# Kernel tuning notes

Measured on AMD Instinct MI355X. Metric: run time of the kernel, lower is better.

Reference implementation:

```python
import jax, jax.numpy as jnp
import numpy as np

B, S, D, H = 2, 2048, 1024, 16
DH = D // H
LEVELS, FACTOR = 3, 2


def setup_inputs() -> dict:
    key = jax.random.key(0)
    ks = jax.random.split(key, 12)
    s = 1.0 / np.sqrt(D)
    n = lambda k, shape, sc: (jax.random.normal(k, shape, jnp.float32) * sc)
    return {
        "query": n(ks[0], (B, S, D), 1.0),
        "key": n(ks[1], (B, S, D), 1.0),
        "value": n(ks[2], (B, S, D), 1.0),
        "Wq": n(ks[3], (D, D), s), "bq": jnp.zeros((D,), jnp.float32),
        "Wk": n(ks[4], (D, D), s), "bk": jnp.zeros((D,), jnp.float32),
        "Wv": n(ks[5], (D, D), s), "bv": jnp.zeros((D,), jnp.float32),
        "Wo": n(ks[6], (D, D), s), "bo": jnp.zeros((D,), jnp.float32),
        "w_levels": jnp.ones((LEVELS,), jnp.float32),
    }


def _downsample(m):
    # mean-pool pairs along sequence: [B, S, D] -> [B, S//FACTOR, D]
    b, s, d = m.shape
    sn = s // FACTOR
    return m[:, : sn * FACTOR, :].reshape(b, sn, FACTOR, d).mean(axis=2)


def _mha(q, k, v, Wq, bq, Wk, bk, Wv, bv, Wo, bo):
    b, sq, d = q.shape
    sk = k.shape[1]
    qh = (q @ Wq + bq).reshape(b, sq, H, DH)
    kh = (k @ Wk + bk).reshape(b, sk, H, DH)
    vh = (v @ Wv + bv).reshape(b, sk, H, DH)
    scores = jnp.einsum("bqhd,bkhd->bhqk", qh, kh) / np.sqrt(DH)
    attn = jax.nn.softmax(scores, axis=-1)
    out = jnp.einsum("bhqk,bkhd->bqhd", attn, vh).reshape(b, sq, d)
    return out @ Wo + bo


def reference(query, key, value, Wq, bq, Wk, bk, Wv, bv, Wo, bo, w_levels):
    keys, vals = [key], [value]
    k_, v_ = key, value
    for _ in range(LEVELS - 1):
        k_ = _downsample(k_)
        v_ = _downsample(v_)
        keys.append(k_)
        vals.append(v_)
    acc = None
    for lvl in range(LEVELS):
        o = _mha(query, keys[lvl], vals[lvl], Wq, bq, Wk, bk, Wv, bv, Wo, bo)
        o = o * w_levels[lvl]
        acc = o if acc is None else acc + o
    return acc / w_levels.sum()
```

## Files before the change

### kernel.cpp

```cpp
#include <hip/hip_runtime.h>


#define B_  2
#define S_  2048
#define D_  1024
#define H_  16
#define DH_ 64
#define THR2 10.0f

typedef short s8v __attribute__((ext_vector_type(8)));
typedef float f4v __attribute__((ext_vector_type(4)));
typedef float f16v __attribute__((ext_vector_type(16)));
typedef unsigned int u32x2 __attribute__((ext_vector_type(2)));
typedef unsigned int u32x4 __attribute__((ext_vector_type(4)));

__device__ __forceinline__ unsigned cvtpk(float lo, float hi){
    unsigned r;
    asm volatile("v_cvt_pk_bf16_f32 %0, %1, %2" : "=v"(r) : "v"(lo), "v"(hi));
    return r;
}
__device__ __forceinline__ unsigned short f2bf1(float v){
    unsigned r;
    asm volatile("v_cvt_pk_bf16_f32 %0, %1, %2" : "=v"(r) : "v"(v), "v"(v));
    return (unsigned short)r;
}
__device__ __forceinline__ float bf2f(unsigned short h){
    union { unsigned u; float f; } v; v.u = ((unsigned)h) << 16;
    return v.f;
}
__device__ __forceinline__ float exp2_(float x){
    float r; asm("v_exp_f32 %0, %1" : "=v"(r) : "v"(x)); return r;
}
__device__ __forceinline__ float max3_(float a, float b, float c){
    float r; asm("v_max3_f32 %0, %1, %2, %3" : "=v"(r) : "v"(a), "v"(b), "v"(c));
    return r;
}
__device__ __forceinline__ void pswap(unsigned &dst, unsigned &src){
    asm volatile("v_permlane32_swap_b32 %0, %1" : "+v"(dst), "+v"(src));
}
__device__ __forceinline__ unsigned addpk3(unsigned x, unsigned y, unsigned z){
    union { unsigned u; float f; } xl, yl, zl, xh, yh, zh;
    xl.u = x << 16;          yl.u = y << 16;          zl.u = z << 16;
    xh.u = x & 0xFFFF0000u;  yh.u = y & 0xFFFF0000u;  zh.u = z & 0xFFFF0000u;
    return cvtpk(xl.f + yl.f + zl.f, xh.f + yh.f + zh.f);
}
__device__ __forceinline__ int swz(int row, int kb){
    return row*128 + (((kb) ^ (row & 7) ^ ((row >> 3) & 7)) << 4);
}
__device__ __forceinline__ void gld16(const void* g, void* l){
    __builtin_amdgcn_global_load_lds(
        (const __attribute__((address_space(1))) unsigned int*)g,
        (__attribute__((address_space(3))) unsigned int*)l, 16, 0, 0);
}

__global__ __launch_bounds__(256) void wtrans(
    const float* __restrict__ W0, const float* __restrict__ W1,
    const float* __restrict__ W2, const float* __restrict__ W3,
    unsigned short* __restrict__ T0, unsigned short* __restrict__ T1,
    unsigned short* __restrict__ T2, unsigned short* __restrict__ T3)
{
    __shared__ float tl[32][33];
    const float* W = blockIdx.z==0?W0: blockIdx.z==1?W1: blockIdx.z==2?W2:W3;
    unsigned short* T = blockIdx.z==0?T0: blockIdx.z==1?T1: blockIdx.z==2?T2:T3;
    const int t = threadIdx.x;
    const int bk = blockIdx.x*32, bn = blockIdx.y*32;
    {
        int row = t>>3, c4 = (t&7)*4;
        float4 v = *(const float4*)&W[(size_t)(bk+row)*D_ + bn + c4];
        tl[row][c4+0]=v.x; tl[row][c4+1]=v.y; tl[row][c4+2]=v.z; tl[row][c4+3]=v.w;
    }
    __syncthreads();
    {
        int n = t>>3, k4 = (t&7)*4;
        unsigned a = cvtpk(tl[k4+0][n], tl[k4+1][n]);
        unsigned b = cvtpk(tl[k4+2][n], tl[k4+3][n]);
        u32x2 pk = {a, b};
        *(u32x2*)&T[(size_t)(bn+n)*D_ + bk + k4] = pk;
    }
}

__global__ __launch_bounds__(256) void gemm_qkv3(
    const float* __restrict__ Aq, const float* __restrict__ Ak, const float* __restrict__ Avv,
    const unsigned short* __restrict__ Wq_, const unsigned short* __restrict__ Wk_,
    const unsigned short* __restrict__ Wv_,
    const float* __restrict__ bq_, const float* __restrict__ bk_, const float* __restrict__ bv_,
    unsigned short* __restrict__ Oq, unsigned short* __restrict__ Ok,
    unsigned short* __restrict__ Ov,
    unsigned short* __restrict__ K1, unsigned short* __restrict__ K2,
    float scale_q)
{
    const int z = blockIdx.z;
    const float* Af = z==0?Aq : z==1?Ak : Avv;
    const unsigned short* Btw = z==0?Wq_ : z==1?Wk_ : Wv_;
    const float* bias = z==0?bq_ : z==1?bk_ : bv_;
    unsigned short* C = z==0?Oq : z==1?Ok : Ov;
    const float scale = z==0? scale_q : 1.0f;

    const int N_ = D_, K_ = D_;
    __shared__ __align__(16) char lds[65536];
    const int t = threadIdx.x;
    const int l = t & 63, wvi = t>>6, g = l>>4, x = l&15;
    const int wr = wvi>>1, wc = wvi&1;
    const int br = blockIdx.x*128, bc = blockIdx.y*128;

    int rw[4], bl[4];
    #pragma unroll
    for (int p=0;p<4;++p){ int u = t + 256*p; rw[p] = u>>3; bl[p] = u&7; }

    f4v acc[4][4];
    #pragma unroll
    for (int i=0;i<4;++i)
        #pragma unroll
        for (int j=0;j<4;++j) acc[i][j] = (f4v){0.f,0.f,0.f,0.f};

    float4 alo[4], ahi[4]; s8v brg[4];
    #pragma unroll
    for (int p=0;p<4;++p){
        const float* ap = Af + (size_t)(br+rw[p])*K_ + bl[p]*8;
        alo[p] = *(const float4*)ap; ahi[p] = *(const float4*)(ap+4);
        brg[p] = *(const s8v*)(Btw + (size_t)(bc+rw[p])*K_ + bl[p]*8);
    }

    int cur = 0;
    for (int kt=0; kt<K_; kt+=64){
        char* AsB = lds + cur*32768;
        char* BsB = AsB + 16384;
        #pragma unroll
        for (int p=0;p<4;++p){
            uint4 pk;
            pk.x = cvtpk(alo[p].x, alo[p].y); pk.y = cvtpk(alo[p].z, alo[p].w);
            pk.z = cvtpk(ahi[p].x, ahi[p].y); pk.w = cvtpk(ahi[p].z, ahi[p].w);
            *(uint4*)(AsB + swz(rw[p], bl[p])) = pk;
            *(s8v*)(BsB + swz(rw[p], bl[p])) = brg[p];
        }
        if (kt + 64 < K_){
            #pragma unroll
            for (int p=0;p<4;++p){
                const float* ap = Af + (size_t)(br+rw[p])*K_ + (kt+64) + bl[p]*8;
                alo[p] = *(const float4*)ap; ahi[p] = *(const float4*)(ap+4);
                brg[p] = *(const s8v*)(Btw + (size_t)(bc+rw[p])*K_ + (kt+64) + bl[p]*8);
            }
        }
        __syncthreads();
        #pragma unroll
        for (int c=0;c<2;++c){
            s8v af[4], bf[4];
            #pragma unroll
            for (int fm=0; fm<4; ++fm)
                af[fm] = *(const s8v*)(AsB + swz(wr*64+fm*16+x, c*4+g));
            #pragma unroll
            for (int fn=0; fn<4; ++fn)
                bf[fn] = *(const s8v*)(BsB + swz(wc*64+fn*16+x, c*4+g));
            __builtin_amdgcn_s_setprio(1);
            #pragma unroll
            for (int fm=0; fm<4; ++fm)
                #pragma unroll
                for (int fn=0; fn<4; ++fn)
                    acc[fm][fn] = __builtin_amdgcn_mfma_f32_16x16x32_bf16(
                        af[fm], bf[fn], acc[fm][fn], 0,0,0);
            __builtin_amdgcn_s_setprio(0);
        }
        cur ^= 1;
    }

    #pragma unroll
    for (int fn=0; fn<4; ++fn){
        int col = bc + wc*64 + fn*16 + x;
        float bv = bias[col];
        #pragma unroll
        for (int fm=0; fm<4; ++fm){
            int row0 = br + wr*64 + fm*16 + g*4;
            float v0 = acc[fm][fn][0] + bv;
            float v1 = acc[fm][fn][1] + bv;
            float v2 = acc[fm][fn][2] + bv;
            float v3 = acc[fm][fn][3] + bv;
            int bI = row0>>11, sI = row0 & (S_-1);
            int hI = col>>6,  dhI = col & (DH_-1);
            size_t bh = (size_t)(bI*H_ + hI);
            if (z != 2){
                unsigned short* p0 = C + (bh*S_ + sI)*DH_ + dhI;
                p0[0]      = f2bf1(v0*scale);
                p0[DH_]    = f2bf1(v1*scale);
                p0[2*DH_]  = f2bf1(v2*scale);
                p0[3*DH_]  = f2bf1(v3*scale);
                if (z == 1){
                    unsigned short* p1 = K1 + (bh*(S_/2) + (sI>>1))*DH_ + dhI;
                    p1[0]   = f2bf1((v0+v1)*0.5f);
                    p1[DH_] = f2bf1((v2+v3)*0.5f);
                    K2[(bh*(S_/4) + (sI>>2))*DH_ + dhI] = f2bf1((v0+v1+v2+v3)*0.25f);
                }
            } else {
                u32x2 pk;
                pk.x = cvtpk(v0, v1);
                pk.y = cvtpk(v2, v3);
                *(u32x2*)&C[(bh*DH_+dhI)*S_ + sI] = pk;
            }
        }
    }
}

__global__ __launch_bounds__(256) void pool_v(
    const unsigned short* __restrict__ V0, unsigned short* __restrict__ V1,
    unsigned short* __restrict__ V2)
{
    int idx = blockIdx.x * 256 + threadIdx.x;
    int row = idx >> 8;
    int c8  = idx & 255;
    union { u32x4 u; unsigned short hh[8]; } a;
    a.u = *(const u32x4*)&V0[((size_t)row << 11) + c8*8];
    float m01 = 0.5f*(bf2f(a.hh[0])+bf2f(a.hh[1]));
    float m23 = 0.5f*(bf2f(a.hh[2])+bf2f(a.hh[3]));
    float m45 = 0.5f*(bf2f(a.hh[4])+bf2f(a.hh[5]));
    float m67 = 0.5f*(bf2f(a.hh[6])+bf2f(a.hh[7]));
    u32x2 p1; p1.x = cvtpk(m01, m23); p1.y = cvtpk(m45, m67);
    *(u32x2*)&V1[((size_t)row << 10) + c8*4] = p1;
    *(unsigned*)&V2[((size_t)row << 9) + c8*2] =
        cvtpk(0.5f*(m01+m23), 0.5f*(m45+m67));
}

__global__ __launch_bounds__(256) void gemm_sum(
    const unsigned short* __restrict__ A0, const unsigned short* __restrict__ A1,
    const unsigned short* __restrict__ A2, const unsigned short* __restrict__ Btw,
    const float* __restrict__ bias, float* __restrict__ C)
{
    const int N_ = D_, K_ = D_;
    __shared__ __align__(16) char lds[49152];
    const int t = threadIdx.x;
    const int l = t & 63, wvi = t>>6, g = l>>4, x = l&15;
    const int wr = wvi>>1, wc = wvi&1;
    const int br = blockIdx.x*128, bc = blockIdx.y*64;

    int rw[4], bl[4];
    #pragma unroll
    for (int p=0;p<4;++p){ int u = t + 256*p; rw[p] = u>>3; bl[p] = u&7; }
    int bw[2], bb[2];
    #pragma unroll
    for (int p=0;p<2;++p){ int u = t + 256*p; bw[p] = u>>3; bb[p] = u&7; }

    f4v acc[4][2];
    #pragma unroll
    for (int i=0;i<4;++i){ acc[i][0] = (f4v){0,0,0,0}; acc[i][1] = (f4v){0,0,0,0}; }

    u32x4 a0r[4], a1r[4], a2r[4]; s8v brg[2];
    #pragma unroll
    for (int p=0;p<4;++p){
        size_t off = (size_t)(br+rw[p])*K_ + bl[p]*8;
        a0r[p] = *(const u32x4*)(A0 + off);
        a1r[p] = *(const u32x4*)(A1 + off);
        a2r[p] = *(const u32x4*)(A2 + off);
    }
    #pragma unroll
    for (int p=0;p<2;++p)
        brg[p] = *(const s8v*)(Btw + (size_t)(bc+bw[p])*K_ + bb[p]*8);

    int cur = 0;
    for (int kt=0; kt<K_; kt+=64){
        char* AsB = lds + cur*24576;
        char* BsB = AsB + 16384;
        #pragma unroll
        for (int p=0;p<4;++p){
            uint4 pk;
            pk.x = addpk3(a0r[p].x, a1r[p].x, a2r[p].x);
            pk.y = addpk3(a0r[p].y, a1r[p].y, a2r[p].y);
            pk.z = addpk3(a0r[p].z, a1r[p].z, a2r[p].z);
            pk.w = addpk3(a0r[p].w, a1r[p].w, a2r[p].w);
            *(uint4*)(AsB + swz(rw[p], bl[p])) = pk;
        }
        #pragma unroll
        for (int p=0;p<2;++p)
            *(s8v*)(BsB + swz(bw[p], bb[p])) = brg[p];
        if (kt + 64 < K_){
            #pragma unroll
            for (int p=0;p<4;++p){
                size_t off = (size_t)(br+rw[p])*K_ + (kt+64) + bl[p]*8;
                a0r[p] = *(const u32x4*)(A0 + off);
                a1r[p] = *(const u32x4*)(A1 + off);
                a2r[p] = *(const u32x4*)(A2 + off);
            }
            #pragma unroll
            for (int p=0;p<2;++p)
                brg[p] = *(const s8v*)(Btw + (size_t)(bc+bw[p])*K_ + (kt+64) + bb[p]*8);
        }
        __syncthreads();
        #pragma unroll
        for (int c=0;c<2;++c){
            s8v af[4], bf[2];
            #pragma unroll
            for (int fm=0; fm<4; ++fm)
                af[fm] = *(const s8v*)(AsB + swz(wr*64+fm*16+x, c*4+g));
            #pragma unroll
            for (int fn=0; fn<2; ++fn)
                bf[fn] = *(const s8v*)(BsB + swz(wc*32+fn*16+x, c*4+g));
            __builtin_amdgcn_s_setprio(1);
            #pragma unroll
            for (int fm=0; fm<4; ++fm)
                #pragma unroll
                for (int fn=0; fn<2; ++fn)
                    acc[fm][fn] = __builtin_amdgcn_mfma_f32_16x16x32_bf16(
                        af[fm], bf[fn], acc[fm][fn], 0,0,0);
            __builtin_amdgcn_s_setprio(0);
        }
        cur ^= 1;
    }

    #pragma unroll
    for (int fn=0; fn<2; ++fn){
        int col = bc + wc*32 + fn*16 + x;
        float bv = bias[col];
        #pragma unroll
        for (int fm=0; fm<4; ++fm){
            int row0 = br + wr*64 + fm*16 + g*4;
            #pragma unroll
            for (int r=0;r<4;++r)
                C[(size_t)(row0+r)*N_ + col] = acc[fm][fn][r] + bv;
        }
    }
}

__global__ __launch_bounds__(256, 4) void attn_mfma11(
    const unsigned short* __restrict__ qh,
    const unsigned short* __restrict__ kh0, const unsigned short* __restrict__ kh1,
    const unsigned short* __restrict__ kh2,
    const unsigned short* __restrict__ vt0, const unsigned short* __restrict__ vt1,
    const unsigned short* __restrict__ vt2,
    const float* __restrict__ wlv,
    unsigned short* __restrict__ acc0, unsigned short* __restrict__ acc1,
    unsigned short* __restrict__ acc2)
{
    __shared__ __align__(16) char ldsA[32768];
    const int t = threadIdx.x, l = t&63, wv = t>>6, q = l&31, hi = l>>5;
    const int bh_ = blockIdx.x;
    const int h = bh_ & (H_-1), b = bh_ >> 4;
    const int qt = blockIdx.y;
    const int lvl = blockIdx.z;
    const int nt = 32 >> lvl;
    const unsigned short* kp  = lvl==0 ? kh0 : (lvl==1 ? kh1 : kh2);
    const unsigned short* vpt = lvl==0 ? vt0 : (lvl==1 ? vt1 : vt2);
    unsigned short* accOut    = lvl==0 ? acc0 : (lvl==1 ? acc1 : acc2);

    const float w0 = wlv[0], w1 = wlv[1], w2 = wlv[2];
    const float wl = wlv[lvl] / (w0 + w1 + w2);

    const unsigned short* qp =
        qh + (((size_t)(b*H_+h))*S_ + (size_t)qt*128 + wv*32 + q)*DH_ + hi*8;
    s8v qf0 = *(const s8v*)(qp);
    s8v qf1 = *(const s8v*)(qp + 16);
    s8v qf2 = *(const s8v*)(qp + 32);
    s8v qf3 = *(const s8v*)(qp + 48);

    const int Sl = nt*64;
    const char* gK = (const char*)(kp + (size_t)(b*H_+h)*Sl*DH_);
    const char* gV = (const char*)(vpt + (size_t)(b*H_+h)*DH_*Sl);

    const int lr = l>>3, lc = l&7;
    const int kb0 = lc ^ lr ^ wv;
    const int kb1 = lc ^ lr ^ (wv+4);
    const int kOffG0 = (((wv*8+lr)*DH_)    + kb0*8)*2;
    const int kOffG1 = (((32+wv*8+lr)*DH_) + kb1*8)*2;
    const int vOffG0 = ((wv*8+lr)*Sl    + kb0*8)*2;
    const int vOffG1 = ((32+wv*8+lr)*Sl + kb1*8)*2;
    const int ldsOff0 = wv*1024, ldsOff1 = 4096 + wv*1024;

    float m_i = -1e30f, l_i = 0.f;
    f16v o0, o1;
    #pragma unroll
    for (int r=0;r<16;++r){ o0[r]=0.f; o1[r]=0.f; }

    {
        char* kB = ldsA;           char* vB = ldsA + 8192;
        gld16(gK + kOffG0, kB + ldsOff0);
        gld16(gK + kOffG1, kB + ldsOff1);
        gld16(gV + vOffG0, vB + ldsOff0);
        gld16(gV + vOffG1, vB + ldsOff1);
    }

    int cur = 0;
    for (int kt = 0; kt < nt; ++kt) {
        asm volatile("s_waitcnt vmcnt(0)" ::: "memory");
        __syncthreads();
        if (kt + 1 < nt) {
            char* kB = ldsA + (cur^1)*16384;
            char* vB = kB + 8192;
            gld16(gK + (size_t)(kt+1)*64*DH_*2 + kOffG0, kB + ldsOff0);
            gld16(gK + (size_t)(kt+1)*64*DH_*2 + kOffG1, kB + ldsOff1);
            gld16(gV + (size_t)(kt+1)*128      + vOffG0, vB + ldsOff0);
            gld16(gV + (size_t)(kt+1)*128      + vOffG1, vB + ldsOff1);
        }
        char* kb_ = ldsA + cur*16384;
        char* vb_ = kb_ + 8192;

        f16v s0, s1;
        #pragma unroll
        for (int r=0;r<16;++r){ s0[r]=0.f; s1[r]=0.f; }
        {
            s8v k00 = *(const s8v*)(kb_ + swz(q,    0*2+hi));
            s8v k01 = *(const s8v*)(kb_ + swz(q,    1*2+hi));
            s8v k10 = *(const s8v*)(kb_ + swz(32+q, 0*2+hi));
            s8v k11 = *(const s8v*)(kb_ + swz(32+q, 1*2+hi));
            __builtin_amdgcn_s_setprio(1);
            s0 = __builtin_amdgcn_mfma_f32_32x32x16_bf16(k00, qf0, s0, 0,0,0);
            s1 = __builtin_amdgcn_mfma_f32_32x32x16_bf16(k10, qf0, s1, 0,0,0);
            s0 = __builtin_amdgcn_mfma_f32_32x32x16_bf16(k01, qf1, s0, 0,0,0);
            s1 = __builtin_amdgcn_mfma_f32_32x32x16_bf16(k11, qf1, s1, 0,0,0);
            __builtin_amdgcn_s_setprio(0);
        }
        {
            s8v k02 = *(const s8v*)(kb_ + swz(q,    2*2+hi));
            s8v k03 = *(const s8v*)(kb_ + swz(q,    3*2+hi));
            s8v k12 = *(const s8v*)(kb_ + swz(32+q, 2*2+hi));
            s8v k13 = *(const s8v*)(kb_ + swz(32+q, 3*2+hi));
            __builtin_amdgcn_s_setprio(1);
            s0 = __builtin_amdgcn_mfma_f32_32x32x16_bf16(k02, qf2, s0, 0,0,0);
            s1 = __builtin_amdgcn_mfma_f32_32x32x16_bf16(k12, qf2, s1, 0,0,0);
            s0 = __builtin_amdgcn_mfma_f32_32x32x16_bf16(k03, qf3, s0, 0,0,0);
            s1 = __builtin_amdgcn_mfma_f32_32x32x16_bf16(k13, qf3, s1, 0,0,0);
            __builtin_amdgcn_s_setprio(0);
        }

        float ca = max3_(s0[0], s0[1], s0[2]);
        ca = max3_(ca, s0[3], s0[4]);
        ca = max3_(ca, s0[5], s0[6]);
        ca = fmaxf(ca, s0[7]);
        float cb = max3_(s0[8], s0[9], s0[10]);
        cb = max3_(cb, s0[11], s0[12]);
        cb = max3_(cb, s0[13], s0[14]);
        cb = fmaxf(cb, s0[15]);
        float cc = max3_(s1[0], s1[1], s1[2]);
        cc = max3_(cc, s1[3], s1[4]);
        cc = max3_(cc, s1[5], s1[6]);
        cc = fmaxf(cc, s1[7]);
        float cd = max3_(s1[8], s1[9], s1[10]);
        cd = max3_(cd, s1[11], s1[12]);
        cd = max3_(cd, s1[13], s1[14]);
        cd = fmaxf(cd, s1[15]);
        float pm = fmaxf(max3_(ca, cb, cc), cd);
        pm = fmaxf(pm, __shfl_xor(pm, 32, 64));
        if (__any(pm > m_i + THR2)) {
            float mn = fmaxf(m_i, pm);
            float corr = exp2_(m_i - mn);
            m_i = mn;
            l_i *= corr;
            #pragma unroll
            for (int r=0;r<16;++r){
                float cbc = __shfl(corr, ((r&3)+8*(r>>2)) + 4*hi, 64);
                o0[r] *= cbc; o1[r] *= cbc;
            }
        }
        float rs = 0.f;
        #pragma unroll
        for (int r=0;r<16;++r){ s0[r] = exp2_(s0[r]-m_i); rs += s0[r]; }
        #pragma unroll
        for (int r=0;r<16;++r){ s1[r] = exp2_(s1[r]-m_i); rs += s1[r]; }
        rs += __shfl_xor(rs, 32, 64);
        l_i += rs;

        unsigned a0 = cvtpk(s0[0], s0[1]),  a1 = cvtpk(s0[2], s0[3]);
        unsigned b0 = cvtpk(s0[4], s0[5]),  b1 = cvtpk(s0[6], s0[7]);
        pswap(a0, b0); pswap(a1, b1);
        unsigned c0 = cvtpk(s0[8], s0[9]),  c1 = cvtpk(s0[10], s0[11]);
        unsigned d0 = cvtpk(s0[12], s0[13]),d1 = cvtpk(s0[14], s0[15]);
        pswap(c0, d0); pswap(c1, d1);
        unsigned e0 = cvtpk(s1[0], s1[1]),  e1 = cvtpk(s1[2], s1[3]);
        unsigned f0 = cvtpk(s1[4], s1[5]),  f1 = cvtpk(s1[6], s1[7]);
        pswap(e0, f0); pswap(e1, f1);
        unsigned g0 = cvtpk(s1[8], s1[9]),  g1 = cvtpk(s1[10], s1[11]);
        unsigned h0 = cvtpk(s1[12], s1[13]),h1 = cvtpk(s1[14], s1[15]);
        pswap(g0, h0); pswap(g1, h1);
        union { u32x4 u; s8v s; } pf0, pf1, pf2, pf3;
        pf0.u = (u32x4){a0, a1, b0, b1};
        pf1.u = (u32x4){c0, c1, d0, d1};
        pf2.u = (u32x4){e0, e1, f0, f1};
        pf3.u = (u32x4){g0, g1, h0, h1};

        {
            s8v v00 = *(const s8v*)(vb_ + swz(q,    0*2+hi));
            s8v v01 = *(const s8v*)(vb_ + swz(q,    1*2+hi));
            s8v v10 = *(const s8v*)(vb_ + swz(32+q, 0*2+hi));
            s8v v11 = *(const s8v*)(vb_ + swz(32+q, 1*2+hi));
            __builtin_amdgcn_s_setprio(1);
            o0 = __builtin_amdgcn_mfma_f32_32x32x16_bf16(pf0.s, v00, o0, 0,0,0);
            o1 = __builtin_amdgcn_mfma_f32_32x32x16_bf16(pf0.s, v10, o1, 0,0,0);
            o0 = __builtin_amdgcn_mfma_f32_32x32x16_bf16(pf1.s, v01, o0, 0,0,0);
            o1 = __builtin_amdgcn_mfma_f32_32x32x16_bf16(pf1.s, v11, o1, 0,0,0);
            __builtin_amdgcn_s_setprio(0);
        }
        {
            s8v v02 = *(const s8v*)(vb_ + swz(q,    2*2+hi));
            s8v v03 = *(const s8v*)(vb_ + swz(q,    3*2+hi));
            s8v v12 = *(const s8v*)(vb_ + swz(32+q, 2*2+hi));
            s8v v13 = *(const s8v*)(vb_ + swz(32+q, 3*2+hi));
            __builtin_amdgcn_s_setprio(1);
            o0 = __builtin_amdgcn_mfma_f32_32x32x16_bf16(pf2.s, v02, o0, 0,0,0);
            o1 = __builtin_amdgcn_mfma_f32_32x32x16_bf16(pf2.s, v12, o1, 0,0,0);
            o0 = __builtin_amdgcn_mfma_f32_32x32x16_bf16(pf3.s, v03, o0, 0,0,0);
            o1 = __builtin_amdgcn_mfma_f32_32x32x16_bf16(pf3.s, v13, o1, 0,0,0);
            __builtin_amdgcn_s_setprio(0);
        }
        cur ^= 1;
    }

    #pragma unroll
    for (int r=0;r<16;++r){
        int qrow = ((r&3)+8*(r>>2)) + 4*hi;
        float lb = __shfl(l_i, qrow, 64);
        float sc = wl / lb;
        size_t row = (size_t)b*S_ + (size_t)qt*128 + wv*32 + qrow;
        accOut[row*D_ + h*DH_ + q]      = f2bf1(o0[r] * sc);
        accOut[row*D_ + h*DH_ + 32 + q] = f2bf1(o1[r] * sc);
    }
}

extern "C" void kernel_launch(void* const* d_in, const int* in_sizes, int n_in,
                              void* d_out, int out_size, void* d_ws, size_t ws_size,
                              hipStream_t stream)
{
    const float* query = (const float*)d_in[0];
    const float* key   = (const float*)d_in[1];
    const float* value = (const float*)d_in[2];
    const float* Wq = (const float*)d_in[3];  const float* bq = (const float*)d_in[4];
    const float* Wk = (const float*)d_in[5];  const float* bk = (const float*)d_in[6];
    const float* Wv = (const float*)d_in[7];  const float* bv = (const float*)d_in[8];
    const float* Wo = (const float*)d_in[9];  const float* bo = (const float*)d_in[10];
    const float* wlv = (const float*)d_in[11];

    char* w = (char*)d_ws;
    unsigned short* qhb  = (unsigned short*)(w);
    unsigned short* khb0 = (unsigned short*)(w + 8388608);
    unsigned short* khb1 = (unsigned short*)(w + 16777216);
    unsigned short* khb2 = (unsigned short*)(w + 20971520);
    unsigned short* vtb0 = (unsigned short*)(w + 23068672);
    unsigned short* vtb1 = (unsigned short*)(w + 31457280);
    unsigned short* vtb2 = (unsigned short*)(w + 35651584);
    unsigned short* Wto  = (unsigned short*)(w + 37748736);
    unsigned short* Wtq  = (unsigned short*)(w + 39845888);
    unsigned short* Wtk  = (unsigned short*)(w + 41943040);
    unsigned short* Wtv  = (unsigned short*)(w + 44040192);
    unsigned short* acc0 = (unsigned short*)(w + 39845888);
    unsigned short* acc1 = (unsigned short*)(w + 48234496);
    unsigned short* acc2 = (unsigned short*)(w + 56623104);

    dim3 bb(256);
    wtrans<<<dim3(32,32,4), bb, 0, stream>>>(Wq, Wk, Wv, Wo, Wtq, Wtk, Wtv, Wto);

    const float scale_q = 0.125f * 1.44269504088896f;
    gemm_qkv3<<<dim3(32, 8, 3), bb, 0, stream>>>(query, key, value,
                                                 Wtq, Wtk, Wtv, bq, bk, bv,
                                                 qhb, khb0, vtb0,
                                                 khb1, khb2, scale_q);

    pool_v<<<2048, bb, 0, stream>>>(vtb0, vtb1, vtb2);

    attn_mfma11<<<dim3(32, 16, 3), bb, 0, stream>>>(qhb, khb0, khb1, khb2,
                                                    vtb0, vtb1, vtb2, wlv,
                                                    acc0, acc1, acc2);

    gemm_sum<<<dim3(32, 16), bb, 0, stream>>>(acc0, acc1, acc2, Wto, bo, (float*)d_out);
}
```

Baseline: 163.7 us.

## Process two query tiles per attention block to reuse staged K/V tiles

Each attention workgroup now handles two 128-row query tiles against every staged K/V tile in LDS, which halves the grid along the query dimension and halves global K/V loads and barriers per query row. The per-tile body is factored into a macro, and the row-sum is rewritten as a tree reduction. In exchange, register pressure roughly doubles for the accumulators, launch bounds drop from 4 to 3 waves per SIMD, and there are fewer blocks (768), which may reduce occupancy and latency hiding.

```diff
diff --git a/kernel.cpp b/kernel.cpp
--- a/kernel.cpp
+++ b/kernel.cpp
@@ -317,7 +317,125 @@
     }
 }
 
-__global__ __launch_bounds__(256, 4) void attn_mfma11(
+#define ATTN_QTILE(QF0,QF1,QF2,QF3,MI,LI,O0,O1)                                   \
+    {                                                                              \
+        f16v s0, s1;                                                               \
+        _Pragma("unroll")                                                          \
+        for (int r=0;r<16;++r){ s0[r]=0.f; s1[r]=0.f; }                            \
+        {                                                                          \
+            s8v k00 = *(const s8v*)(kb_ + swz(q,    0*2+hi));                      \
+            s8v k01 = *(const s8v*)(kb_ + swz(q,    1*2+hi));                      \
+            s8v k10 = *(const s8v*)(kb_ + swz(32+q, 0*2+hi));                      \
+            s8v k11 = *(const s8v*)(kb_ + swz(32+q, 1*2+hi));                      \
+            __builtin_amdgcn_s_setprio(1);                                         \
+            s0 = __builtin_amdgcn_mfma_f32_32x32x16_bf16(k00, QF0, s0, 0,0,0);     \
+            s1 = __builtin_amdgcn_mfma_f32_32x32x16_bf16(k10, QF0, s1, 0,0,0);     \
+            s0 = __builtin_amdgcn_mfma_f32_32x32x16_bf16(k01, QF1, s0, 0,0,0);     \
+            s1 = __builtin_amdgcn_mfma_f32_32x32x16_bf16(k11, QF1, s1, 0,0,0);     \
+            __builtin_amdgcn_s_setprio(0);                                         \
+        }                                                                          \
+        {                                                                          \
+            s8v k02 = *(const s8v*)(kb_ + swz(q,    2*2+hi));                      \
+            s8v k03 = *(const s8v*)(kb_ + swz(q,    3*2+hi));                      \
+            s8v k12 = *(const s8v*)(kb_ + swz(32+q, 2*2+hi));                      \
+            s8v k13 = *(const s8v*)(kb_ + swz(32+q, 3*2+hi));                      \
+            __builtin_amdgcn_s_setprio(1);                                         \
+            s0 = __builtin_amdgcn_mfma_f32_32x32x16_bf16(k02, QF2, s0, 0,0,0);     \
+            s1 = __builtin_amdgcn_mfma_f32_32x32x16_bf16(k12, QF2, s1, 0,0,0);     \
+            s0 = __builtin_amdgcn_mfma_f32_32x32x16_bf16(k03, QF3, s0, 0,0,0);     \
+            s1 = __builtin_amdgcn_mfma_f32_32x32x16_bf16(k13, QF3, s1, 0,0,0);     \
+            __builtin_amdgcn_s_setprio(0);                                         \
+        }                                                                          \
+        float ca = max3_(s0[0], s0[1], s0[2]);                                     \
+        ca = max3_(ca, s0[3], s0[4]);                                              \
+        ca = max3_(ca, s0[5], s0[6]);                                              \
+        ca = fmaxf(ca, s0[7]);                                                     \
+        float cb = max3_(s0[8], s0[9], s0[10]);                                    \
+        cb = max3_(cb, s0[11], s0[12]);                                            \
+        cb = max3_(cb, s0[13], s0[14]);                                            \
+        cb = fmaxf(cb, s0[15]);                                                    \
+        float cc = max3_(s1[0], s1[1], s1[2]);                                     \
+        cc = max3_(cc, s1[3], s1[4]);                                              \
+        cc = max3_(cc, s1[5], s1[6]);                                              \
+        cc = fmaxf(cc, s1[7]);                                                     \
+        float cd = max3_(s1[8], s1[9], s1[10]);                                    \
+        cd = max3_(cd, s1[11], s1[12]);                                            \
+        cd = max3_(cd, s1[13], s1[14]);                                            \
+        cd = fmaxf(cd, s1[15]);                                                    \
+        float pm = fmaxf(max3_(ca, cb, cc), cd);                                   \
+        pm = fmaxf(pm, __shfl_xor(pm, 32, 64));                                    \
+        if (__any(pm > MI + THR2)) {                                               \
+            float mn = fmaxf(MI, pm);                                              \
+            float corr = exp2_(MI - mn);                                           \
+            MI = mn;                                                               \
+            LI *= corr;                                                            \
+            _Pragma("unroll")                                                      \
+            for (int r=0;r<16;++r){                                                \
+                float cbc = __shfl(corr, ((r&3)+8*(r>>2)) + 4*hi, 64);             \
+                O0[r] *= cbc; O1[r] *= cbc;                                        \
+            }                                                                      \
+        }                                                                          \
+        _Pragma("unroll")                                                          \
+        for (int r=0;r<16;++r) s0[r] = exp2_(s0[r]-MI);                            \
+        _Pragma("unroll")                                                          \
+        for (int r=0;r<16;++r) s1[r] = exp2_(s1[r]-MI);                            \
+        {                                                                          \
+            float r0 = s0[0]+s0[4],  r1 = s0[1]+s0[5];                             \
+            float r2 = s0[2]+s0[6],  r3 = s0[3]+s0[7];                             \
+            float r4 = s1[0]+s1[4],  r5 = s1[1]+s1[5];                             \
+            float r6 = s1[2]+s1[6],  r7 = s1[3]+s1[7];                             \
+            r0 += s0[8]+s0[12];  r1 += s0[9]+s0[13];                               \
+            r2 += s0[10]+s0[14]; r3 += s0[11]+s0[15];                              \
+            r4 += s1[8]+s1[12];  r5 += s1[9]+s1[13];                               \
+            r6 += s1[10]+s1[14]; r7 += s1[11]+s1[15];                              \
+            float rs = ((r0+r1)+(r2+r3)) + ((r4+r5)+(r6+r7));                      \
+            rs += __shfl_xor(rs, 32, 64);                                          \
+            LI += rs;                                                              \
+        }                                                                          \
+        unsigned a0 = cvtpk(s0[0], s0[1]),  a1 = cvtpk(s0[2], s0[3]);              \
+        unsigned b0 = cvtpk(s0[4], s0[5]),  b1 = cvtpk(s0[6], s0[7]);              \
+        pswap(a0, b0); pswap(a1, b1);                                              \
+        unsigned c0 = cvtpk(s0[8], s0[9]),  c1 = cvtpk(s0[10], s0[11]);            \
+        unsigned d0 = cvtpk(s0[12], s0[13]),d1 = cvtpk(s0[14], s0[15]);            \
+        pswap(c0, d0); pswap(c1, d1);                                              \
+        unsigned e0 = cvtpk(s1[0], s1[1]),  e1 = cvtpk(s1[2], s1[3]);              \
+        unsigned f0 = cvtpk(s1[4], s1[5]),  f1 = cvtpk(s1[6], s1[7]);              \
+        pswap(e0, f0); pswap(e1, f1);                                              \
+        unsigned g0 = cvtpk(s1[8], s1[9]),  g1 = cvtpk(s1[10], s1[11]);            \
+        unsigned h0 = cvtpk(s1[12], s1[13]),h1 = cvtpk(s1[14], s1[15]);            \
+        pswap(g0, h0); pswap(g1, h1);                                              \
+        union { u32x4 u; s8v s; } pf0, pf1, pf2, pf3;                              \
+        pf0.u = (u32x4){a0, a1, b0, b1};                                           \
+        pf1.u = (u32x4){c0, c1, d0, d1};                                           \
+        pf2.u = (u32x4){e0, e1, f0, f1};                                           \
+        pf3.u = (u32x4){g0, g1, h0, h1};                                           \
+        {                                                                          \
+            s8v v00 = *(const s8v*)(vb_ + swz(q,    0*2+hi));                      \
+            s8v v01 = *(const s8v*)(vb_ + swz(q,    1*2+hi));                      \
+            s8v v10 = *(const s8v*)(vb_ + swz(32+q, 0*2+hi));                      \
+            s8v v11 = *(const s8v*)(vb_ + swz(32+q, 1*2+hi));                      \
+            __builtin_amdgcn_s_setprio(1);                                         \
+            O0 = __builtin_amdgcn_mfma_f32_32x32x16_bf16(pf0.s, v00, O0, 0,0,0);   \
+            O1 = __builtin_amdgcn_mfma_f32_32x32x16_bf16(pf0.s, v10, O1, 0,0,0);   \
+            O0 = __builtin_amdgcn_mfma_f32_32x32x16_bf16(pf1.s, v01, O0, 0,0,0);   \
+            O1 = __builtin_amdgcn_mfma_f32_32x32x16_bf16(pf1.s, v11, O1, 0,0,0);   \
+            __builtin_amdgcn_s_setprio(0);                                         \
+        }                                                                          \
+        {                                                                          \
+            s8v v02 = *(const s8v*)(vb_ + swz(q,    2*2+hi));                      \
+            s8v v03 = *(const s8v*)(vb_ + swz(q,    3*2+hi));                      \
+            s8v v12 = *(const s8v*)(vb_ + swz(32+q, 2*2+hi));                      \
+            s8v v13 = *(const s8v*)(vb_ + swz(32+q, 3*2+hi));                      \
+            __builtin_amdgcn_s_setprio(1);                                         \
+            O0 = __builtin_amdgcn_mfma_f32_32x32x16_bf16(pf2.s, v02, O0, 0,0,0);   \
+            O1 = __builtin_amdgcn_mfma_f32_32x32x16_bf16(pf2.s, v12, O1, 0,0,0);   \
+            O0 = __builtin_amdgcn_mfma_f32_32x32x16_bf16(pf3.s, v03, O0, 0,0,0);   \
+            O1 = __builtin_amdgcn_mfma_f32_32x32x16_bf16(pf3.s, v13, O1, 0,0,0);   \
+            __builtin_amdgcn_s_setprio(0);                                         \
+        }                                                                          \
+    }
+
+__global__ __launch_bounds__(256, 3) void attn_mfma15(
     const unsigned short* __restrict__ qh,
     const unsigned short* __restrict__ kh0, const unsigned short* __restrict__ kh1,
     const unsigned short* __restrict__ kh2,
@@ -331,7 +449,7 @@
     const int t = threadIdx.x, l = t&63, wv = t>>6, q = l&31, hi = l>>5;
     const int bh_ = blockIdx.x;
     const int h = bh_ & (H_-1), b = bh_ >> 4;
-    const int qt = blockIdx.y;
+    const int qtA = blockIdx.y*2, qtB = qtA + 1;
     const int lvl = blockIdx.z;
     const int nt = 32 >> lvl;
     const unsigned short* kp  = lvl==0 ? kh0 : (lvl==1 ? kh1 : kh2);
@@ -341,12 +459,17 @@
     const float w0 = wlv[0], w1 = wlv[1], w2 = wlv[2];
     const float wl = wlv[lvl] / (w0 + w1 + w2);
 
-    const unsigned short* qp =
-        qh + (((size_t)(b*H_+h))*S_ + (size_t)qt*128 + wv*32 + q)*DH_ + hi*8;
-    s8v qf0 = *(const s8v*)(qp);
-    s8v qf1 = *(const s8v*)(qp + 16);
-    s8v qf2 = *(const s8v*)(qp + 32);
-    s8v qf3 = *(const s8v*)(qp + 48);
+    const unsigned short* qpA =
+        qh + (((size_t)(b*H_+h))*S_ + (size_t)qtA*128 + wv*32 + q)*DH_ + hi*8;
+    s8v qfA0 = *(const s8v*)(qpA);
+    s8v qfA1 = *(const s8v*)(qpA + 16);
+    s8v qfA2 = *(const s8v*)(qpA + 32);
+    s8v qfA3 = *(const s8v*)(qpA + 48);
+    const unsigned short* qpB = qpA + (size_t)128*DH_;
+    s8v qfB0 = *(const s8v*)(qpB);
+    s8v qfB1 = *(const s8v*)(qpB + 16);
+    s8v qfB2 = *(const s8v*)(qpB + 32);
+    s8v qfB3 = *(const s8v*)(qpB + 48);
 
     const int Sl = nt*64;
     const char* gK = (const char*)(kp + (size_t)(b*H_+h)*Sl*DH_);
@@ -361,10 +484,10 @@
     const int vOffG1 = ((32+wv*8+lr)*Sl + kb1*8)*2;
     const int ldsOff0 = wv*1024, ldsOff1 = 4096 + wv*1024;
 
-    float m_i = -1e30f, l_i = 0.f;
-    f16v o0, o1;
-    #pragma unroll
-    for (int r=0;r<16;++r){ o0[r]=0.f; o1[r]=0.f; }
+    float mA = -1e30f, lA = 0.f, mB = -1e30f, lB = 0.f;
+    f16v oA0, oA1, oB0, oB1;
+    #pragma unroll
+    for (int r=0;r<16;++r){ oA0[r]=0.f; oA1[r]=0.f; oB0[r]=0.f; oB1[r]=0.f; }
 
     {
         char* kB = ldsA;           char* vB = ldsA + 8192;
@@ -389,124 +512,25 @@
         char* kb_ = ldsA + cur*16384;
         char* vb_ = kb_ + 8192;
 
-        f16v s0, s1;
-        #pragma unroll
-        for (int r=0;r<16;++r){ s0[r]=0.f; s1[r]=0.f; }
-        {
-            s8v k00 = *(const s8v*)(kb_ + swz(q,    0*2+hi));
-            s8v k01 = *(const s8v*)(kb_ + swz(q,    1*2+hi));
-            s8v k10 = *(const s8v*)(kb_ + swz(32+q, 0*2+hi));
-            s8v k11 = *(const s8v*)(kb_ + swz(32+q, 1*2+hi));
-            __builtin_amdgcn_s_setprio(1);
-            s0 = __builtin_amdgcn_mfma_f32_32x32x16_bf16(k00, qf0, s0, 0,0,0);
-            s1 = __builtin_amdgcn_mfma_f32_32x32x16_bf16(k10, qf0, s1, 0,0,0);
-            s0 = __builtin_amdgcn_mfma_f32_32x32x16_bf16(k01, qf1, s0, 0,0,0);
-            s1 = __builtin_amdgcn_mfma_f32_32x32x16_bf16(k11, qf1, s1, 0,0,0);
-            __builtin_amdgcn_s_setprio(0);
-        }
-        {
-            s8v k02 = *(const s8v*)(kb_ + swz(q,    2*2+hi));
-            s8v k03 = *(const s8v*)(kb_ + swz(q,    3*2+hi));
-            s8v k12 = *(const s8v*)(kb_ + swz(32+q, 2*2+hi));
-            s8v k13 = *(const s8v*)(kb_ + swz(32+q, 3*2+hi));
-            __builtin_amdgcn_s_setprio(1);
-            s0 = __builtin_amdgcn_mfma_f32_32x32x16_bf16(k02, qf2, s0, 0,0,0);
-            s1 = __builtin_amdgcn_mfma_f32_32x32x16_bf16(k12, qf2, s1, 0,0,0);
-            s0 = __builtin_amdgcn_mfma_f32_32x32x16_bf16(k03, qf3, s0, 0,0,0);
-            s1 = __builtin_amdgcn_mfma_f32_32x32x16_bf16(k13, qf3, s1, 0,0,0);
-            __builtin_amdgcn_s_setprio(0);
-        }
-
-        float ca = max3_(s0[0], s0[1], s0[2]);
-        ca = max3_(ca, s0[3], s0[4]);
-        ca = max3_(ca, s0[5], s0[6]);
-        ca = fmaxf(ca, s0[7]);
-        float cb = max3_(s0[8], s0[9], s0[10]);
-        cb = max3_(cb, s0[11], s0[12]);
-        cb = max3_(cb, s0[13], s0[14]);
-        cb = fmaxf(cb, s0[15]);
-        float cc = max3_(s1[0], s1[1], s1[2]);
-        cc = max3_(cc, s1[3], s1[4]);
-        cc = max3_(cc, s1[5], s1[6]);
-        cc = fmaxf(cc, s1[7]);
-        float cd = max3_(s1[8], s1[9], s1[10]);
-        cd = max3_(cd, s1[11], s1[12]);
-        cd = max3_(cd, s1[13], s1[14]);
-        cd = fmaxf(cd, s1[15]);
-        float pm = fmaxf(max3_(ca, cb, cc), cd);
-        pm = fmaxf(pm, __shfl_xor(pm, 32, 64));
-        if (__any(pm > m_i + THR2)) {
-            float mn = fmaxf(m_i, pm);
-            float corr = exp2_(m_i - mn);
-            m_i = mn;
-            l_i *= corr;
-            #pragma unroll
-            for (int r=0;r<16;++r){
-                float cbc = __shfl(corr, ((r&3)+8*(r>>2)) + 4*hi, 64);
-                o0[r] *= cbc; o1[r] *= cbc;
-            }
-        }
-        float rs = 0.f;
-        #pragma unroll
-        for (int r=0;r<16;++r){ s0[r] = exp2_(s0[r]-m_i); rs += s0[r]; }
-        #pragma unroll
-        for (int r=0;r<16;++r){ s1[r] = exp2_(s1[r]-m_i); rs += s1[r]; }
-        rs += __shfl_xor(rs, 32, 64);
-        l_i += rs;
-
-        unsigned a0 = cvtpk(s0[0], s0[1]),  a1 = cvtpk(s0[2], s0[3]);
-        unsigned b0 = cvtpk(s0[4], s0[5]),  b1 = cvtpk(s0[6], s0[7]);
-        pswap(a0, b0); pswap(a1, b1);
-        unsigned c0 = cvtpk(s0[8], s0[9]),  c1 = cvtpk(s0[10], s0[11]);
-        unsigned d0 = cvtpk(s0[12], s0[13]),d1 = cvtpk(s0[14], s0[15]);
-        pswap(c0, d0); pswap(c1, d1);
-        unsigned e0 = cvtpk(s1[0], s1[1]),  e1 = cvtpk(s1[2], s1[3]);
-        unsigned f0 = cvtpk(s1[4], s1[5]),  f1 = cvtpk(s1[6], s1[7]);
-        pswap(e0, f0); pswap(e1, f1);
-        unsigned g0 = cvtpk(s1[8], s1[9]),  g1 = cvtpk(s1[10], s1[11]);
-        unsigned h0 = cvtpk(s1[12], s1[13]),h1 = cvtpk(s1[14], s1[15]);
-        pswap(g0, h0); pswap(g1, h1);
-        union { u32x4 u; s8v s; } pf0, pf1, pf2, pf3;
-        pf0.u = (u32x4){a0, a1, b0, b1};
-        pf1.u = (u32x4){c0, c1, d0, d1};
-        pf2.u = (u32x4){e0, e1, f0, f1};
-        pf3.u = (u32x4){g0, g1, h0, h1};
-
-        {
-            s8v v00 = *(const s8v*)(vb_ + swz(q,    0*2+hi));
-            s8v v01 = *(const s8v*)(vb_ + swz(q,    1*2+hi));
-            s8v v10 = *(const s8v*)(vb_ + swz(32+q, 0*2+hi));
-            s8v v11 = *(const s8v*)(vb_ + swz(32+q, 1*2+hi));
-            __builtin_amdgcn_s_setprio(1);
-            o0 = __builtin_amdgcn_mfma_f32_32x32x16_bf16(pf0.s, v00, o0, 0,0,0);
-            o1 = __builtin_amdgcn_mfma_f32_32x32x16_bf16(pf0.s, v10, o1, 0,0,0);
-            o0 = __builtin_amdgcn_mfma_f32_32x32x16_bf16(pf1.s, v01, o0, 0,0,0);
-            o1 = __builtin_amdgcn_mfma_f32_32x32x16_bf16(pf1.s, v11, o1, 0,0,0);
-            __builtin_amdgcn_s_setprio(0);
-        }
-        {
-            s8v v02 = *(const s8v*)(vb_ + swz(q,    2*2+hi));
-            s8v v03 = *(const s8v*)(vb_ + swz(q,    3*2+hi));
-            s8v v12 = *(const s8v*)(vb_ + swz(32+q, 2*2+hi));
-            s8v v13 = *(const s8v*)(vb_ + swz(32+q, 3*2+hi));
-            __builtin_amdgcn_s_setprio(1);
-            o0 = __builtin_amdgcn_mfma_f32_32x32x16_bf16(pf2.s, v02, o0, 0,0,0);
-            o1 = __builtin_amdgcn_mfma_f32_32x32x16_bf16(pf2.s, v12, o1, 0,0,0);
-            o0 = __builtin_amdgcn_mfma_f32_32x32x16_bf16(pf3.s, v03, o0, 0,0,0);
-            o1 = __builtin_amdgcn_mfma_f32_32x32x16_bf16(pf3.s, v13, o1, 0,0,0);
-            __builtin_amdgcn_s_setprio(0);
-        }
+        ATTN_QTILE(qfA0,qfA1,qfA2,qfA3, mA, lA, oA0, oA1)
+        ATTN_QTILE(qfB0,qfB1,qfB2,qfB3, mB, lB, oB0, oB1)
+
         cur ^= 1;
     }
 
     #pragma unroll
     for (int r=0;r<16;++r){
         int qrow = ((r&3)+8*(r>>2)) + 4*hi;
-        float lb = __shfl(l_i, qrow, 64);
-        float sc = wl / lb;
-        size_t row = (size_t)b*S_ + (size_t)qt*128 + wv*32 + qrow;
-        accOut[row*D_ + h*DH_ + q]      = f2bf1(o0[r] * sc);
-        accOut[row*D_ + h*DH_ + 32 + q] = f2bf1(o1[r] * sc);
+        float lbA = __shfl(lA, qrow, 64);
+        float scA = wl / lbA;
+        size_t rowA = (size_t)b*S_ + (size_t)qtA*128 + wv*32 + qrow;
+        accOut[rowA*D_ + h*DH_ + q]      = f2bf1(oA0[r] * scA);
+        accOut[rowA*D_ + h*DH_ + 32 + q] = f2bf1(oA1[r] * scA);
+        float lbB = __shfl(lB, qrow, 64);
+        float scB = wl / lbB;
+        size_t rowB = rowA + 128;
+        accOut[rowB*D_ + h*DH_ + q]      = f2bf1(oB0[r] * scB);
+        accOut[rowB*D_ + h*DH_ + 32 + q] = f2bf1(oB1[r] * scB);
     }
 }
 
@@ -550,9 +574,9 @@
 
     pool_v<<<2048, bb, 0, stream>>>(vtb0, vtb1, vtb2);
 
-    attn_mfma11<<<dim3(32, 16, 3), bb, 0, stream>>>(qhb, khb0, khb1, khb2,
-                                                    vtb0, vtb1, vtb2, wlv,
-                                                    acc0, acc1, acc2);
+    attn_mfma15<<<dim3(32, 8, 3), bb, 0, stream>>>(qhb, khb0, khb1, khb2,
+                                                   vtb0, vtb1, vtb2, wlv,
+                                                   acc0, acc1, acc2);
 
     gemm_sum<<<dim3(32, 16), bb, 0, stream>>>(acc0, acc1, acc2, Wto, bo, (float*)d_out);
 }
```

Result: slower. 176.9 us (+8.1%).
